# Kernel tuning notes

Measured on AMD Instinct MI355X. Metric: run time of the kernel, lower is better.

Reference implementation:

```python
import jax, jax.numpy as jnp
import numpy as np

NUM_EXPERTS = 12
TOP_K = 2
FFN_DIM = 1280
HIDDEN = 2048


def setup_inputs() -> dict:
    key = jax.random.key(0)
    k0, k1, k2, k3, k4 = jax.random.split(key, 5)
    B, S, H, F, E = 4, 1024, HIDDEN, FFN_DIM, NUM_EXPERTS
    hidden_states = jax.random.normal(k0, (B, S, H), dtype=jnp.float32)
    # single gate actually used (cluster_index_count=0 -> cluster_index_list[-1])
    gate_w = jax.random.normal(k1, (E, H), dtype=jnp.float32) * 0.02
    w1 = jax.random.normal(k2, (E, F, H), dtype=jnp.float32) * 0.02  # f1: H->F
    w2 = jax.random.normal(k3, (E, H, F), dtype=jnp.float32) * 0.02  # f2: F->H
    w3 = jax.random.normal(k4, (E, F, H), dtype=jnp.float32) * 0.02  # f3: H->F
    return {"hidden_states": hidden_states, "gate_w": gate_w, "w1": w1, "w2": w2, "w3": w3}


def reference(hidden_states, gate_w, w1, w2, w3):
    B, S, H = hidden_states.shape
    x = hidden_states.reshape(-1, H)                       # [T, H]
    T = x.shape[0]
    logits = x @ gate_w.T                                  # [T, E]
    probs = jax.nn.softmax(logits, axis=-1)
    top_w, top_i = jax.lax.top_k(probs, TOP_K)             # [T, 2]
    top_w = top_w / jnp.sum(top_w, axis=-1, keepdims=True)
    # dense combine weights [T, E]: routing weight if expert selected else 0
    cw = jnp.zeros((T, NUM_EXPERTS), dtype=x.dtype)
    cw = cw.at[jnp.arange(T)[:, None], top_i].add(top_w)
    out = jnp.zeros_like(x)
    for e in range(NUM_EXPERTS):  # fixed small expert loop
        h = jax.nn.silu(x @ w1[e].T) * (x @ w3[e].T)       # SwiGLU [T, F]
        out = out + (h @ w2[e].T) * cw[:, e:e + 1]
    return out.reshape(B, S, H)
```

## Files before the change

### kernel.cpp

```cpp
#include <hip/hip_runtime.h>

#define T_TOK 4096
#define H_DIM 2048
#define F_DIM 1280
#define NE 12
#define TOTAL_ROWS (2 * T_TOK)

typedef float f32x4 __attribute__((ext_vector_type(4)));
typedef short bf16x8 __attribute__((ext_vector_type(8)));

__device__ __forceinline__ unsigned short f2bf(float f) {
    unsigned int u = __float_as_uint(f);
    u += 0x7FFFu + ((u >> 16) & 1u);
    return (unsigned short)(u >> 16);
}

__device__ __forceinline__ void gl2lds16(const void* g, void* l) {
    __builtin_amdgcn_global_load_lds(
        (const __attribute__((address_space(1))) unsigned int*)g,
        (__attribute__((address_space(3))) unsigned int*)l,
        16, 0, 0);
}

__global__ __launch_bounds__(256) void convert_kernel(
    const float* __restrict__ src, unsigned short* __restrict__ dst)
{
    size_t i = ((size_t)blockIdx.x * 256 + threadIdx.x) * 8;
    float4 a = *(const float4*)(src + i);
    float4 b = *(const float4*)(src + i + 4);
    unsigned short o[8];
    o[0] = f2bf(a.x); o[1] = f2bf(a.y); o[2] = f2bf(a.z); o[3] = f2bf(a.w);
    o[4] = f2bf(b.x); o[5] = f2bf(b.y); o[6] = f2bf(b.z); o[7] = f2bf(b.w);
    *(uint4*)(dst + i) = *(const uint4*)o;
}

__global__ __launch_bounds__(256) void gate_kernel(
    const float* __restrict__ x, const float* __restrict__ gw,
    int* __restrict__ counts, int* __restrict__ top_e, float* __restrict__ top_w)
{
    int gid = blockIdx.x * blockDim.x + threadIdx.x;
    int tok = gid >> 6;
    int lane = threadIdx.x & 63;
    if (tok >= T_TOK) return;
    const float* xr = x + (size_t)tok * H_DIM;
    float4 xs[8];
#pragma unroll
    for (int c = 0; c < 8; ++c) xs[c] = *(const float4*)(xr + c * 256 + lane * 4);
    float acc[NE];
#pragma unroll
    for (int e = 0; e < NE; ++e) {
        const float* gr = gw + (size_t)e * H_DIM;
        float s = 0.f;
#pragma unroll
        for (int c = 0; c < 8; ++c) {
            float4 g = *(const float4*)(gr + c * 256 + lane * 4);
            s += xs[c].x * g.x + xs[c].y * g.y + xs[c].z * g.z + xs[c].w * g.w;
        }
        acc[e] = s;
    }
#pragma unroll
    for (int e = 0; e < NE; ++e) {
#pragma unroll
        for (int off = 32; off > 0; off >>= 1)
            acc[e] += __shfl_xor(acc[e], off, 64);
    }
    if (lane == 0) {
        int b0 = 0;
#pragma unroll
        for (int e = 1; e < NE; ++e) if (acc[e] > acc[b0]) b0 = e;
        int b1 = (b0 == 0) ? 1 : 0;
#pragma unroll
        for (int e = 0; e < NE; ++e) if (e != b0 && acc[e] > acc[b1]) b1 = e;
        float t = __expf(acc[b1] - acc[b0]);
        float w0 = 1.f / (1.f + t);
        top_e[tok * 2] = b0; top_e[tok * 2 + 1] = b1;
        top_w[tok * 2] = w0; top_w[tok * 2 + 1] = 1.f - w0;
        atomicAdd(&counts[b0], 1);
        atomicAdd(&counts[b1], 1);
    }
}

__global__ void scan_kernel(const int* __restrict__ counts, int* __restrict__ offsets,
                            int* __restrict__ cursors)
{
    if (threadIdx.x == 0 && blockIdx.x == 0) {
        int s = 0;
        for (int e = 0; e < NE; ++e) { offsets[e] = s; s += counts[e]; cursors[e] = 0; }
        offsets[NE] = s;
    }
}

__global__ __launch_bounds__(256) void scatter_kernel(
    const int* __restrict__ top_e, const float* __restrict__ top_w,
    const int* __restrict__ offsets, int* __restrict__ cursors,
    int* __restrict__ row_token, float* __restrict__ row_weight,
    int* __restrict__ inv_pos)
{
    int t = blockIdx.x * blockDim.x + threadIdx.x;
    if (t >= T_TOK) return;
#pragma unroll
    for (int s = 0; s < 2; ++s) {
        int e = top_e[t * 2 + s];
        int pos = atomicAdd(&cursors[e], 1);
        int r = offsets[e] + pos;
        row_token[r] = t;
        row_weight[r] = top_w[t * 2 + s];
        inv_pos[t * 2 + s] = r;
    }
}

__global__ __launch_bounds__(256) void ffn1_kernel(
    const unsigned short* __restrict__ xb, const unsigned short* __restrict__ w1b,
    const unsigned short* __restrict__ w3b,
    const int* __restrict__ counts, const int* __restrict__ offsets,
    const int* __restrict__ row_token, unsigned short* __restrict__ hbuf)
{
    int e = blockIdx.z;
    int cnt = counts[e];
    int m0 = blockIdx.y * 128;
    if (m0 >= cnt) return;
    int base = offsets[e];
    int n0 = blockIdx.x * 128;

    __shared__ unsigned short As[128 * 32];
    __shared__ unsigned short B1s[128 * 32];
    __shared__ unsigned short B3s[128 * 32];

    int t = threadIdx.x;
    int lane = t & 63;
    int wid = t >> 6;
    int wm = wid >> 1, wn = wid & 1;
    int lr = lane & 15, lq = lane >> 4;

    int srow = t >> 2;
    int chunk = t & 3;
    int tok0 = row_token[base + min(m0 + srow, cnt - 1)];
    int tok1 = row_token[base + min(m0 + 64 + srow, cnt - 1)];
    const unsigned short* gA0 = xb + (size_t)tok0 * H_DIM + chunk * 8;
    const unsigned short* gA1 = xb + (size_t)tok1 * H_DIM + chunk * 8;
    const unsigned short* gB1 = w1b + ((size_t)e * F_DIM + n0 + srow) * H_DIM + chunk * 8;
    const unsigned short* gB3 = w3b + ((size_t)e * F_DIM + n0 + srow) * H_DIM + chunk * 8;
    const size_t rowskip = (size_t)64 * H_DIM;

    unsigned short* lA0 = As + wid * 512;
    unsigned short* lA1 = As + 2048 + wid * 512;
    unsigned short* lB10 = B1s + wid * 512;
    unsigned short* lB11 = B1s + 2048 + wid * 512;
    unsigned short* lB30 = B3s + wid * 512;
    unsigned short* lB31 = B3s + 2048 + wid * 512;

    f32x4 acc1[4][4] = {};
    f32x4 acc3[4][4] = {};

    for (int k0 = 0; k0 < H_DIM; k0 += 32) {
        gl2lds16(gA0 + k0, lA0);
        gl2lds16(gA1 + k0, lA1);
        gl2lds16(gB1 + k0, lB10);
        gl2lds16(gB1 + rowskip + k0, lB11);
        gl2lds16(gB3 + k0, lB30);
        gl2lds16(gB3 + rowskip + k0, lB31);
        __syncthreads();

        bf16x8 af[4];
#pragma unroll
        for (int ms = 0; ms < 4; ++ms)
            af[ms] = *(const bf16x8*)(As + (wm * 64 + ms * 16 + lr) * 32 + lq * 8);
#pragma unroll
        for (int ns = 0; ns < 4; ++ns) {
            bf16x8 b1 = *(const bf16x8*)(B1s + (wn * 64 + ns * 16 + lr) * 32 + lq * 8);
            bf16x8 b3 = *(const bf16x8*)(B3s + (wn * 64 + ns * 16 + lr) * 32 + lq * 8);
#pragma unroll
            for (int ms = 0; ms < 4; ++ms) {
                acc1[ms][ns] = __builtin_amdgcn_mfma_f32_16x16x32_bf16(af[ms], b1, acc1[ms][ns], 0, 0, 0);
                acc3[ms][ns] = __builtin_amdgcn_mfma_f32_16x16x32_bf16(af[ms], b3, acc3[ms][ns], 0, 0, 0);
            }
        }
        __syncthreads();
    }

#pragma unroll
    for (int ms = 0; ms < 4; ++ms) {
#pragma unroll
        for (int i = 0; i < 4; ++i) {
            int r = wm * 64 + ms * 16 + lq * 4 + i;
            if (m0 + r < cnt) {
                size_t rowoff = (size_t)(base + m0 + r) * F_DIM;
#pragma unroll
                for (int ns = 0; ns < 4; ++ns) {
                    int c = n0 + wn * 64 + ns * 16 + lr;
                    float a = acc1[ms][ns][i];
                    float hv = (a / (1.f + __expf(-a))) * acc3[ms][ns][i];
                    hbuf[rowoff + c] = f2bf(hv);
                }
            }
        }
    }
}

__global__ __launch_bounds__(256) void ffn2_kernel(
    const unsigned short* __restrict__ hbuf, const unsigned short* __restrict__ w2b,
    const int* __restrict__ counts, const int* __restrict__ offsets,
    const float* __restrict__ row_weight, float* __restrict__ ybuf)
{
    int e = blockIdx.z;
    int cnt = counts[e];
    int m0 = blockIdx.y * 128;
    if (m0 >= cnt) return;
    int base = offsets[e];
    int n0 = blockIdx.x * 128;

    __shared__ unsigned short As[128 * 32];
    __shared__ unsigned short Bs[128 * 32];

    int t = threadIdx.x;
    int lane = t & 63;
    int wid = t >> 6;
    int wm = wid >> 1, wn = wid & 1;
    int lr = lane & 15, lq = lane >> 4;

    int srow = t >> 2;
    int chunk = t & 3;
    const unsigned short* gA0 = hbuf + (size_t)(base + min(m0 + srow, cnt - 1)) * F_DIM + chunk * 8;
    const unsigned short* gA1 = hbuf + (size_t)(base + min(m0 + 64 + srow, cnt - 1)) * F_DIM + chunk * 8;
    const unsigned short* gB = w2b + ((size_t)e * H_DIM + n0 + srow) * F_DIM + chunk * 8;
    const size_t rowskip = (size_t)64 * F_DIM;

    unsigned short* lA0 = As + wid * 512;
    unsigned short* lA1 = As + 2048 + wid * 512;
    unsigned short* lB0 = Bs + wid * 512;
    unsigned short* lB1 = Bs + 2048 + wid * 512;

    f32x4 acc[4][4] = {};

    for (int k0 = 0; k0 < F_DIM; k0 += 32) {
        gl2lds16(gA0 + k0, lA0);
        gl2lds16(gA1 + k0, lA1);
        gl2lds16(gB + k0, lB0);
        gl2lds16(gB + rowskip + k0, lB1);
        __syncthreads();

        bf16x8 af[4];
#pragma unroll
        for (int ms = 0; ms < 4; ++ms)
            af[ms] = *(const bf16x8*)(As + (wm * 64 + ms * 16 + lr) * 32 + lq * 8);
#pragma unroll
        for (int ns = 0; ns < 4; ++ns) {
            bf16x8 b = *(const bf16x8*)(Bs + (wn * 64 + ns * 16 + lr) * 32 + lq * 8);
#pragma unroll
            for (int ms = 0; ms < 4; ++ms)
                acc[ms][ns] = __builtin_amdgcn_mfma_f32_16x16x32_bf16(af[ms], b, acc[ms][ns], 0, 0, 0);
        }
        __syncthreads();
    }

#pragma unroll
    for (int ms = 0; ms < 4; ++ms) {
#pragma unroll
        for (int i = 0; i < 4; ++i) {
            int r = wm * 64 + ms * 16 + lq * 4 + i;
            if (m0 + r < cnt) {
                float wgt = row_weight[base + m0 + r];
                size_t rowoff = (size_t)(base + m0 + r) * H_DIM;
#pragma unroll
                for (int ns = 0; ns < 4; ++ns) {
                    int c = n0 + wn * 64 + ns * 16 + lr;
                    ybuf[rowoff + c] = acc[ms][ns][i] * wgt;
                }
            }
        }
    }
}

__global__ __launch_bounds__(256) void combine_kernel(
    const float* __restrict__ ybuf, const int* __restrict__ inv_pos,
    float* __restrict__ out)
{
    int tk = blockIdx.x;
    int p0 = inv_pos[2 * tk];
    int p1 = inv_pos[2 * tk + 1];
    const float4* y0 = (const float4*)(ybuf + (size_t)p0 * H_DIM);
    const float4* y1 = (const float4*)(ybuf + (size_t)p1 * H_DIM);
    float4* o = (float4*)(out + (size_t)tk * H_DIM);
#pragma unroll
    for (int i = threadIdx.x; i < H_DIM / 4; i += 256) {
        float4 a = y0[i], b = y1[i];
        float4 r;
        r.x = a.x + b.x; r.y = a.y + b.y; r.z = a.z + b.z; r.w = a.w + b.w;
        o[i] = r;
    }
}

extern "C" void kernel_launch(void* const* d_in, const int* in_sizes, int n_in,
                              void* d_out, int out_size, void* d_ws, size_t ws_size,
                              hipStream_t stream)
{
    const float* x  = (const float*)d_in[0];
    const float* gw = (const float*)d_in[1];
    const float* w1 = (const float*)d_in[2];
    const float* w2 = (const float*)d_in[3];
    const float* w3 = (const float*)d_in[4];
    float* out = (float*)d_out;

    unsigned char* p = (unsigned char*)d_ws;
    int* counts     = (int*)p;  p += 256;
    int* cursors    = (int*)p;  p += 256;
    int* offsets    = (int*)p;  p += 256;
    int* top_e      = (int*)p;  p += 2 * T_TOK * 4;
    float* top_w    = (float*)p; p += 2 * T_TOK * 4;
    int* row_token  = (int*)p;  p += 2 * T_TOK * 4;
    float* row_weight = (float*)p; p += 2 * T_TOK * 4;
    int* inv_pos    = (int*)p;  p += 2 * T_TOK * 4;
    unsigned short* xb  = (unsigned short*)p; p += (size_t)T_TOK * H_DIM * 2;
    unsigned short* w2b = (unsigned short*)p; p += (size_t)NE * H_DIM * F_DIM * 2;
    unsigned short* hb  = (unsigned short*)p; p += (size_t)TOTAL_ROWS * F_DIM * 2;
    unsigned short* w1b = (unsigned short*)p;
    unsigned short* w3b = (unsigned short*)(p + (size_t)NE * F_DIM * H_DIM * 2);
    float* ybuf = (float*)p;

    const int WELEM = NE * F_DIM * H_DIM;
    convert_kernel<<<T_TOK * H_DIM / 2048, 256, 0, stream>>>(x, xb);
    convert_kernel<<<WELEM / 2048, 256, 0, stream>>>(w1, w1b);
    convert_kernel<<<WELEM / 2048, 256, 0, stream>>>(w2, w2b);
    convert_kernel<<<WELEM / 2048, 256, 0, stream>>>(w3, w3b);

    hipMemsetAsync(counts, 0, 64 * sizeof(int), stream);
    gate_kernel<<<T_TOK / 4, 256, 0, stream>>>(x, gw, counts, top_e, top_w);
    scan_kernel<<<1, 64, 0, stream>>>(counts, offsets, cursors);
    scatter_kernel<<<T_TOK / 256, 256, 0, stream>>>(top_e, top_w, offsets, cursors,
                                                    row_token, row_weight, inv_pos);

    dim3 g1(F_DIM / 128, 32, NE);
    ffn1_kernel<<<g1, 256, 0, stream>>>(xb, w1b, w3b, counts, offsets, row_token, hb);

    dim3 g2(H_DIM / 128, 32, NE);
    ffn2_kernel<<<g2, 256, 0, stream>>>(hb, w2b, counts, offsets, row_weight, ybuf);

    combine_kernel<<<T_TOK, 256, 0, stream>>>(ybuf, inv_pos, out);
}
```

Measured before the change: 839.8 us.

## Fuse fp32 weight conversion into expert GEMMs with persistent M loop and swizzled LDS

Drops the three separate weight fp32->bf16 conversion passes. The FFN1 and FFN2 kernels now load fp32 weights directly, convert them in registers and store them into an XOR-swizzled LDS tile with K=64. The grids are reshaped so each block walks several M tiles of its expert, with blocks sharing one (n, expert) slot strided by 1024 rows. This removes the extra write and read of about 190MB of converted weights. In exchange, fp32 weight traffic into the GEMM doubles and is repeated for every M tile, with no double buffering to overlap the conversion.

```diff
diff --git a/kernel.cpp b/kernel.cpp
--- a/kernel.cpp
+++ b/kernel.cpp
@@ -1,10 +1,10 @@
 #include <hip/hip_runtime.h>
+#include <hip/hip_bf16.h>
 
 #define T_TOK 4096
 #define H_DIM 2048
 #define F_DIM 1280
 #define NE 12
-#define TOTAL_ROWS (2 * T_TOK)
 
 typedef float f32x4 __attribute__((ext_vector_type(4)));
 typedef short bf16x8 __attribute__((ext_vector_type(8)));
@@ -13,6 +13,11 @@
     unsigned int u = __float_as_uint(f);
     u += 0x7FFFu + ((u >> 16) & 1u);
     return (unsigned short)(u >> 16);
+}
+
+__device__ __forceinline__ unsigned int f2bf2(float lo, float hi) {
+    __hip_bfloat162 p = __float22bfloat162_rn(make_float2(lo, hi));
+    return *(unsigned int*)&p;
 }
 
 __device__ __forceinline__ void gl2lds16(const void* g, void* l) {
@@ -28,9 +33,9 @@
     size_t i = ((size_t)blockIdx.x * 256 + threadIdx.x) * 8;
     float4 a = *(const float4*)(src + i);
     float4 b = *(const float4*)(src + i + 4);
-    unsigned short o[8];
-    o[0] = f2bf(a.x); o[1] = f2bf(a.y); o[2] = f2bf(a.z); o[3] = f2bf(a.w);
-    o[4] = f2bf(b.x); o[5] = f2bf(b.y); o[6] = f2bf(b.z); o[7] = f2bf(b.w);
+    unsigned int o[4];
+    o[0] = f2bf2(a.x, a.y); o[1] = f2bf2(a.z, a.w);
+    o[2] = f2bf2(b.x, b.y); o[3] = f2bf2(b.z, b.w);
     *(uint4*)(dst + i) = *(const uint4*)o;
 }
 
@@ -109,22 +114,23 @@
     }
 }
 
-__global__ __launch_bounds__(256) void ffn1_kernel(
-    const unsigned short* __restrict__ xb, const unsigned short* __restrict__ w1b,
-    const unsigned short* __restrict__ w3b,
+__global__ __launch_bounds__(256, 3) void ffn1_kernel(
+    const unsigned short* __restrict__ xb, const float* __restrict__ w1,
+    const float* __restrict__ w3,
     const int* __restrict__ counts, const int* __restrict__ offsets,
     const int* __restrict__ row_token, unsigned short* __restrict__ hbuf)
 {
     int e = blockIdx.z;
+    int n_blk = blockIdx.y;
+    if (((blockIdx.x ^ (e * 20 + n_blk)) & 7) != 0) return;
+    int m_slot = blockIdx.x >> 3;
     int cnt = counts[e];
-    int m0 = blockIdx.y * 128;
-    if (m0 >= cnt) return;
+    if (m_slot * 128 >= cnt) return;
     int base = offsets[e];
-    int n0 = blockIdx.x * 128;
-
-    __shared__ unsigned short As[128 * 32];
-    __shared__ unsigned short B1s[128 * 32];
-    __shared__ unsigned short B3s[128 * 32];
+    int n0 = n_blk * 64;
+
+    __shared__ unsigned short As[128 * 64];
+    __shared__ unsigned short Bs[128 * 64];
 
     int t = threadIdx.x;
     int lane = t & 63;
@@ -132,85 +138,112 @@
     int wm = wid >> 1, wn = wid & 1;
     int lr = lane & 15, lq = lane >> 4;
 
-    int srow = t >> 2;
-    int chunk = t & 3;
-    int tok0 = row_token[base + min(m0 + srow, cnt - 1)];
-    int tok1 = row_token[base + min(m0 + 64 + srow, cnt - 1)];
-    const unsigned short* gA0 = xb + (size_t)tok0 * H_DIM + chunk * 8;
-    const unsigned short* gA1 = xb + (size_t)tok1 * H_DIM + chunk * 8;
-    const unsigned short* gB1 = w1b + ((size_t)e * F_DIM + n0 + srow) * H_DIM + chunk * 8;
-    const unsigned short* gB3 = w3b + ((size_t)e * F_DIM + n0 + srow) * H_DIM + chunk * 8;
-    const size_t rowskip = (size_t)64 * H_DIM;
-
-    unsigned short* lA0 = As + wid * 512;
-    unsigned short* lA1 = As + 2048 + wid * 512;
-    unsigned short* lB10 = B1s + wid * 512;
-    unsigned short* lB11 = B1s + 2048 + wid * 512;
-    unsigned short* lB30 = B3s + wid * 512;
-    unsigned short* lB31 = B3s + 2048 + wid * 512;
-
-    f32x4 acc1[4][4] = {};
-    f32x4 acc3[4][4] = {};
-
-    for (int k0 = 0; k0 < H_DIM; k0 += 32) {
-        gl2lds16(gA0 + k0, lA0);
-        gl2lds16(gA1 + k0, lA1);
-        gl2lds16(gB1 + k0, lB10);
-        gl2lds16(gB1 + rowskip + k0, lB11);
-        gl2lds16(gB3 + k0, lB30);
-        gl2lds16(gB3 + rowskip + k0, lB31);
-        __syncthreads();
-
-        bf16x8 af[4];
-#pragma unroll
-        for (int ms = 0; ms < 4; ++ms)
-            af[ms] = *(const bf16x8*)(As + (wm * 64 + ms * 16 + lr) * 32 + lq * 8);
-#pragma unroll
-        for (int ns = 0; ns < 4; ++ns) {
-            bf16x8 b1 = *(const bf16x8*)(B1s + (wn * 64 + ns * 16 + lr) * 32 + lq * 8);
-            bf16x8 b3 = *(const bf16x8*)(B3s + (wn * 64 + ns * 16 + lr) * 32 + lq * 8);
-#pragma unroll
-            for (int ms = 0; ms < 4; ++ms) {
-                acc1[ms][ns] = __builtin_amdgcn_mfma_f32_16x16x32_bf16(af[ms], b1, acc1[ms][ns], 0, 0, 0);
-                acc3[ms][ns] = __builtin_amdgcn_mfma_f32_16x16x32_bf16(af[ms], b3, acc3[ms][ns], 0, 0, 0);
-            }
-        }
-        __syncthreads();
-    }
-
-#pragma unroll
-    for (int ms = 0; ms < 4; ++ms) {
+    int brow = t >> 1;
+    int bc0 = (t & 1) * 4;
+    const float* bRowPtr = (brow < 64)
+        ? (w1 + ((size_t)e * F_DIM + n0 + brow) * H_DIM + bc0 * 8)
+        : (w3 + ((size_t)e * F_DIM + (n0 + brow - 64)) * H_DIM + bc0 * 8);
+    unsigned short* bWr[4];
+#pragma unroll
+    for (int j = 0; j < 4; ++j)
+        bWr[j] = Bs + brow * 64 + ((bc0 + j) ^ (brow & 7)) * 8;
+
+    const int aoff = (((t & 7) ^ ((t >> 3) & 7))) * 8;
+    unsigned short* aDst[4];
+#pragma unroll
+    for (int i = 0; i < 4; ++i) aDst[i] = As + i * 2048 + wid * 512 + lane * 8;
+
+    const int po0 = ((0 + lq) ^ (lr & 7)) * 8;
+    const int po1 = ((4 + lq) ^ (lr & 7)) * 8;
+
+    for (int m0 = m_slot * 128; m0 < cnt; m0 += 1024) {
+        const unsigned short* aPtr[4];
 #pragma unroll
         for (int i = 0; i < 4; ++i) {
-            int r = wm * 64 + ms * 16 + lq * 4 + i;
-            if (m0 + r < cnt) {
-                size_t rowoff = (size_t)(base + m0 + r) * F_DIM;
-#pragma unroll
-                for (int ns = 0; ns < 4; ++ns) {
-                    int c = n0 + wn * 64 + ns * 16 + lr;
-                    float a = acc1[ms][ns][i];
-                    float hv = (a / (1.f + __expf(-a))) * acc3[ms][ns][i];
-                    hbuf[rowoff + c] = f2bf(hv);
+            int r = i * 32 + (t >> 3);
+            int tok = row_token[base + min(m0 + r, cnt - 1)];
+            aPtr[i] = xb + (size_t)tok * H_DIM + aoff;
+        }
+        f32x4 acc1[4][2] = {};
+        f32x4 acc3[4][2] = {};
+
+        for (int k0 = 0; k0 < H_DIM; k0 += 64) {
+#pragma unroll
+            for (int i = 0; i < 4; ++i) gl2lds16(aPtr[i] + k0, aDst[i]);
+#pragma unroll
+            for (int h = 0; h < 2; ++h) {
+                float4 v0 = *(const float4*)(bRowPtr + k0 + h * 16);
+                float4 v1 = *(const float4*)(bRowPtr + k0 + h * 16 + 4);
+                float4 v2 = *(const float4*)(bRowPtr + k0 + h * 16 + 8);
+                float4 v3 = *(const float4*)(bRowPtr + k0 + h * 16 + 12);
+                unsigned int o0[4], o1[4];
+                o0[0] = f2bf2(v0.x, v0.y); o0[1] = f2bf2(v0.z, v0.w);
+                o0[2] = f2bf2(v1.x, v1.y); o0[3] = f2bf2(v1.z, v1.w);
+                o1[0] = f2bf2(v2.x, v2.y); o1[1] = f2bf2(v2.z, v2.w);
+                o1[2] = f2bf2(v3.x, v3.y); o1[3] = f2bf2(v3.z, v3.w);
+                *(uint4*)bWr[2 * h]     = *(const uint4*)o0;
+                *(uint4*)bWr[2 * h + 1] = *(const uint4*)o1;
+            }
+            __syncthreads();
+#pragma unroll
+            for (int s = 0; s < 2; ++s) {
+                int po = s ? po1 : po0;
+                bf16x8 af[4], b1f[2], b3f[2];
+#pragma unroll
+                for (int ms = 0; ms < 4; ++ms)
+                    af[ms] = *(const bf16x8*)(As + (wm * 64 + ms * 16 + lr) * 64 + po);
+#pragma unroll
+                for (int ns = 0; ns < 2; ++ns) {
+                    b1f[ns] = *(const bf16x8*)(Bs + (wn * 32 + ns * 16 + lr) * 64 + po);
+                    b3f[ns] = *(const bf16x8*)(Bs + (64 + wn * 32 + ns * 16 + lr) * 64 + po);
                 }
-            }
-        }
-    }
-}
-
-__global__ __launch_bounds__(256) void ffn2_kernel(
-    const unsigned short* __restrict__ hbuf, const unsigned short* __restrict__ w2b,
+#pragma unroll
+                for (int ms = 0; ms < 4; ++ms)
+#pragma unroll
+                    for (int ns = 0; ns < 2; ++ns) {
+                        acc1[ms][ns] = __builtin_amdgcn_mfma_f32_16x16x32_bf16(af[ms], b1f[ns], acc1[ms][ns], 0, 0, 0);
+                        acc3[ms][ns] = __builtin_amdgcn_mfma_f32_16x16x32_bf16(af[ms], b3f[ns], acc3[ms][ns], 0, 0, 0);
+                    }
+            }
+            __syncthreads();
+        }
+
+#pragma unroll
+        for (int ms = 0; ms < 4; ++ms) {
+#pragma unroll
+            for (int i = 0; i < 4; ++i) {
+                int r = wm * 64 + ms * 16 + lq * 4 + i;
+                if (m0 + r < cnt) {
+                    size_t rowoff = (size_t)(base + m0 + r) * F_DIM;
+#pragma unroll
+                    for (int ns = 0; ns < 2; ++ns) {
+                        int c = n0 + wn * 32 + ns * 16 + lr;
+                        float a = acc1[ms][ns][i];
+                        float hv = (a / (1.f + __expf(-a))) * acc3[ms][ns][i];
+                        hbuf[rowoff + c] = f2bf(hv);
+                    }
+                }
+            }
+        }
+    }
+}
+
+__global__ __launch_bounds__(256, 3) void ffn2_kernel(
+    const unsigned short* __restrict__ hbuf, const float* __restrict__ w2,
     const int* __restrict__ counts, const int* __restrict__ offsets,
     const float* __restrict__ row_weight, float* __restrict__ ybuf)
 {
     int e = blockIdx.z;
+    int n_blk = blockIdx.y;
+    if (((blockIdx.x ^ (e * 16 + n_blk)) & 7) != 0) return;
+    int m_slot = blockIdx.x >> 3;
     int cnt = counts[e];
-    int m0 = blockIdx.y * 128;
-    if (m0 >= cnt) return;
+    if (m_slot * 128 >= cnt) return;
     int base = offsets[e];
-    int n0 = blockIdx.x * 128;
-
-    __shared__ unsigned short As[128 * 32];
-    __shared__ unsigned short Bs[128 * 32];
+    int n0 = n_blk * 128;
+
+    __shared__ unsigned short As[128 * 64];
+    __shared__ unsigned short Bs[128 * 64];
 
     int t = threadIdx.x;
     int lane = t & 63;
@@ -218,53 +251,81 @@
     int wm = wid >> 1, wn = wid & 1;
     int lr = lane & 15, lq = lane >> 4;
 
-    int srow = t >> 2;
-    int chunk = t & 3;
-    const unsigned short* gA0 = hbuf + (size_t)(base + min(m0 + srow, cnt - 1)) * F_DIM + chunk * 8;
-    const unsigned short* gA1 = hbuf + (size_t)(base + min(m0 + 64 + srow, cnt - 1)) * F_DIM + chunk * 8;
-    const unsigned short* gB = w2b + ((size_t)e * H_DIM + n0 + srow) * F_DIM + chunk * 8;
-    const size_t rowskip = (size_t)64 * F_DIM;
-
-    unsigned short* lA0 = As + wid * 512;
-    unsigned short* lA1 = As + 2048 + wid * 512;
-    unsigned short* lB0 = Bs + wid * 512;
-    unsigned short* lB1 = Bs + 2048 + wid * 512;
-
-    f32x4 acc[4][4] = {};
-
-    for (int k0 = 0; k0 < F_DIM; k0 += 32) {
-        gl2lds16(gA0 + k0, lA0);
-        gl2lds16(gA1 + k0, lA1);
-        gl2lds16(gB + k0, lB0);
-        gl2lds16(gB + rowskip + k0, lB1);
-        __syncthreads();
-
-        bf16x8 af[4];
-#pragma unroll
-        for (int ms = 0; ms < 4; ++ms)
-            af[ms] = *(const bf16x8*)(As + (wm * 64 + ms * 16 + lr) * 32 + lq * 8);
-#pragma unroll
-        for (int ns = 0; ns < 4; ++ns) {
-            bf16x8 b = *(const bf16x8*)(Bs + (wn * 64 + ns * 16 + lr) * 32 + lq * 8);
-#pragma unroll
-            for (int ms = 0; ms < 4; ++ms)
-                acc[ms][ns] = __builtin_amdgcn_mfma_f32_16x16x32_bf16(af[ms], b, acc[ms][ns], 0, 0, 0);
-        }
-        __syncthreads();
-    }
-
-#pragma unroll
-    for (int ms = 0; ms < 4; ++ms) {
+    int brow = t >> 1;
+    int bc0 = (t & 1) * 4;
+    const float* bRowPtr = w2 + ((size_t)e * H_DIM + n0 + brow) * F_DIM + bc0 * 8;
+    unsigned short* bWr[4];
+#pragma unroll
+    for (int j = 0; j < 4; ++j)
+        bWr[j] = Bs + brow * 64 + ((bc0 + j) ^ (brow & 7)) * 8;
+
+    const int aoff = (((t & 7) ^ ((t >> 3) & 7))) * 8;
+    unsigned short* aDst[4];
+#pragma unroll
+    for (int i = 0; i < 4; ++i) aDst[i] = As + i * 2048 + wid * 512 + lane * 8;
+
+    const int po0 = ((0 + lq) ^ (lr & 7)) * 8;
+    const int po1 = ((4 + lq) ^ (lr & 7)) * 8;
+
+    for (int m0 = m_slot * 128; m0 < cnt; m0 += 1024) {
+        const unsigned short* aPtr[4];
 #pragma unroll
         for (int i = 0; i < 4; ++i) {
-            int r = wm * 64 + ms * 16 + lq * 4 + i;
-            if (m0 + r < cnt) {
-                float wgt = row_weight[base + m0 + r];
-                size_t rowoff = (size_t)(base + m0 + r) * H_DIM;
-#pragma unroll
-                for (int ns = 0; ns < 4; ++ns) {
-                    int c = n0 + wn * 64 + ns * 16 + lr;
-                    ybuf[rowoff + c] = acc[ms][ns][i] * wgt;
+            int r = i * 32 + (t >> 3);
+            aPtr[i] = hbuf + (size_t)(base + min(m0 + r, cnt - 1)) * F_DIM + aoff;
+        }
+        f32x4 acc[4][4] = {};
+
+        for (int k0 = 0; k0 < F_DIM; k0 += 64) {
+#pragma unroll
+            for (int i = 0; i < 4; ++i) gl2lds16(aPtr[i] + k0, aDst[i]);
+#pragma unroll
+            for (int h = 0; h < 2; ++h) {
+                float4 v0 = *(const float4*)(bRowPtr + k0 + h * 16);
+                float4 v1 = *(const float4*)(bRowPtr + k0 + h * 16 + 4);
+                float4 v2 = *(const float4*)(bRowPtr + k0 + h * 16 + 8);
+                float4 v3 = *(const float4*)(bRowPtr + k0 + h * 16 + 12);
+                unsigned int o0[4], o1[4];
+                o0[0] = f2bf2(v0.x, v0.y); o0[1] = f2bf2(v0.z, v0.w);
+                o0[2] = f2bf2(v1.x, v1.y); o0[3] = f2bf2(v1.z, v1.w);
+                o1[0] = f2bf2(v2.x, v2.y); o1[1] = f2bf2(v2.z, v2.w);
+                o1[2] = f2bf2(v3.x, v3.y); o1[3] = f2bf2(v3.z, v3.w);
+                *(uint4*)bWr[2 * h]     = *(const uint4*)o0;
+                *(uint4*)bWr[2 * h + 1] = *(const uint4*)o1;
+            }
+            __syncthreads();
+#pragma unroll
+            for (int s = 0; s < 2; ++s) {
+                int po = s ? po1 : po0;
+                bf16x8 af[4], bf[4];
+#pragma unroll
+                for (int ms = 0; ms < 4; ++ms)
+                    af[ms] = *(const bf16x8*)(As + (wm * 64 + ms * 16 + lr) * 64 + po);
+#pragma unroll
+                for (int ns = 0; ns < 4; ++ns)
+                    bf[ns] = *(const bf16x8*)(Bs + (wn * 64 + ns * 16 + lr) * 64 + po);
+#pragma unroll
+                for (int ms = 0; ms < 4; ++ms)
+#pragma unroll
+                    for (int ns = 0; ns < 4; ++ns)
+                        acc[ms][ns] = __builtin_amdgcn_mfma_f32_16x16x32_bf16(af[ms], bf[ns], acc[ms][ns], 0, 0, 0);
+            }
+            __syncthreads();
+        }
+
+#pragma unroll
+        for (int ms = 0; ms < 4; ++ms) {
+#pragma unroll
+            for (int i = 0; i < 4; ++i) {
+                int r = wm * 64 + ms * 16 + lq * 4 + i;
+                if (m0 + r < cnt) {
+                    float wgt = row_weight[base + m0 + r];
+                    size_t rowoff = (size_t)(base + m0 + r) * H_DIM;
+#pragma unroll
+                    for (int ns = 0; ns < 4; ++ns) {
+                        int c = n0 + wn * 64 + ns * 16 + lr;
+                        ybuf[rowoff + c] = acc[ms][ns][i] * wgt;
+                    }
                 }
             }
         }
@@ -310,18 +371,11 @@
     int* row_token  = (int*)p;  p += 2 * T_TOK * 4;
     float* row_weight = (float*)p; p += 2 * T_TOK * 4;
     int* inv_pos    = (int*)p;  p += 2 * T_TOK * 4;
-    unsigned short* xb  = (unsigned short*)p; p += (size_t)T_TOK * H_DIM * 2;
-    unsigned short* w2b = (unsigned short*)p; p += (size_t)NE * H_DIM * F_DIM * 2;
-    unsigned short* hb  = (unsigned short*)p; p += (size_t)TOTAL_ROWS * F_DIM * 2;
-    unsigned short* w1b = (unsigned short*)p;
-    unsigned short* w3b = (unsigned short*)(p + (size_t)NE * F_DIM * H_DIM * 2);
+    unsigned short* xb = (unsigned short*)p; p += (size_t)T_TOK * H_DIM * 2;
+    unsigned short* hb = (unsigned short*)p; p += (size_t)2 * T_TOK * F_DIM * 2;
     float* ybuf = (float*)p;
 
-    const int WELEM = NE * F_DIM * H_DIM;
     convert_kernel<<<T_TOK * H_DIM / 2048, 256, 0, stream>>>(x, xb);
-    convert_kernel<<<WELEM / 2048, 256, 0, stream>>>(w1, w1b);
-    convert_kernel<<<WELEM / 2048, 256, 0, stream>>>(w2, w2b);
-    convert_kernel<<<WELEM / 2048, 256, 0, stream>>>(w3, w3b);
 
     hipMemsetAsync(counts, 0, 64 * sizeof(int), stream);
     gate_kernel<<<T_TOK / 4, 256, 0, stream>>>(x, gw, counts, top_e, top_w);
@@ -329,11 +383,11 @@
     scatter_kernel<<<T_TOK / 256, 256, 0, stream>>>(top_e, top_w, offsets, cursors,
                                                     row_token, row_weight, inv_pos);
 
-    dim3 g1(F_DIM / 128, 32, NE);
-    ffn1_kernel<<<g1, 256, 0, stream>>>(xb, w1b, w3b, counts, offsets, row_token, hb);
-
-    dim3 g2(H_DIM / 128, 32, NE);
-    ffn2_kernel<<<g2, 256, 0, stream>>>(hb, w2b, counts, offsets, row_weight, ybuf);
+    dim3 g1(64, F_DIM / 64, NE);
+    ffn1_kernel<<<g1, 256, 0, stream>>>(xb, w1, w3, counts, offsets, row_token, hb);
+
+    dim3 g2(64, H_DIM / 128, NE);
+    ffn2_kernel<<<g2, 256, 0, stream>>>(hb, w2, counts, offsets, row_weight, ybuf);
 
     combine_kernel<<<T_TOK, 256, 0, stream>>>(ybuf, inv_pos, out);
 }
```

Measured after the change: 911.5 us. 8.5% more time.
